# Kernel optimization log

Measured on AMD Instinct MI355X. Metric: run time of the kernel, lower is better.

## Reference

```python
import jax, jax.numpy as jnp
import numpy as np

OUT_HW = 224  # fixed by the dilation tensor built inside forward
K = 3         # kernel size


def _axis_terms(coords, size):
    """Bilinear interpolation terms along one axis.
    coords: float coordinates, any shape. Returns clipped int neighbor
    indices (i0, i1) and weights (w0, w1) with zero weight outside [0, size)."""
    c0 = jnp.floor(coords)
    f = coords - c0
    i0 = c0.astype(jnp.int32)
    i1 = i0 + 1
    w0 = (1.0 - f) * ((i0 >= 0) & (i0 < size)).astype(coords.dtype)
    w1 = f * ((i1 >= 0) & (i1 < size)).astype(coords.dtype)
    return jnp.clip(i0, 0, size - 1), jnp.clip(i1, 0, size - 1), w0, w1


def setup_inputs() -> dict:
    key = jax.random.key(0)
    k1, k2, k3 = jax.random.split(key, 3)
    B, C, H, W = 16, 3, 1024, 1024
    x = jax.random.normal(k1, (B, C, H, W), dtype=jnp.float32)
    # normalized sample coordinates in [-1, 1] per output row / column
    stride_h = jax.random.uniform(k2, (B, OUT_HW), dtype=jnp.float32, minval=-1.0, maxval=1.0)
    stride_w = jax.random.uniform(k3, (B, OUT_HW), dtype=jnp.float32, minval=-1.0, maxval=1.0)
    # fixed identity weight from __init__: center tap on channel diagonal
    w = np.zeros((3, 3, K, K), dtype=np.float32)
    for c in range(3):
        w[c, c, 1, 1] = 1.0
    return {"x": x, "stride_h": stride_h, "stride_w": stride_w, "weight": jnp.asarray(w)}


def reference(x, stride_h, stride_w, weight):
    B, C, H, W = x.shape
    dt = x.dtype
    # map normalized [-1,1] coords to pixel coords (as in forward)
    ch = (stride_h + 1.0) * (H - 1) * 0.5            # [B, outH]
    cw = (stride_w + 1.0) * (W - 1) * 0.5            # [B, outW]
    offs = (jnp.arange(K, dtype=dt) - (K - 1) / 2)   # dilation == 1 (built as ones in forward)
    ys = ch[:, :, None] + offs                       # [B, outH, K]
    xs = cw[:, :, None] + offs                       # [B, outW, K]

    yi0, yi1, wy0, wy1 = _axis_terms(ys, H)
    xi0, xi1, wx0, wx1 = _axis_terms(xs, W)

    # gather rows: [B, C, outH, K, W]
    gat_h = jax.vmap(lambda xb, idx: xb[:, idx, :])
    row = (wy0[:, None, :, :, None] * gat_h(x, yi0)
           + wy1[:, None, :, :, None] * gat_h(x, yi1))
    # gather cols: [B, C, outH, Kh, outW, Kw]
    gat_w = jax.vmap(lambda rb, idx: rb[..., idx])
    samp = (wx0[:, None, None, None] * gat_w(row, xi0)
            + wx1[:, None, None, None] * gat_w(row, xi1))
    # contract with (fixed) kernel: out[b,o,i,j]
    return jnp.einsum('bciujv,ocuv->boij', samp, weight)
```

## Files before the change

kernel.cpp:

```cpp
#include <hip/hip_runtime.h>

#define OH 224
#define OW 224
#define HH 1024
#define WW 1024
#define HW (HH * WW)

typedef __attribute__((address_space(3))) void lds_void_t;
typedef const __attribute__((address_space(1))) void g_void_t;

__global__ __launch_bounds__(256) void adaptive_sam_kernel(
    const float* __restrict__ x,
    const float* __restrict__ sh,
    const float* __restrict__ sw,
    const float* __restrict__ wgt,
    float* __restrict__ out,
    int B)
{
    __shared__ float lds[3 * 4 * WW];
    __shared__ float ws[81];

    const int tid = threadIdx.x;
    const int bi  = blockIdx.x;
    const int i   = bi % OH;
    const int b   = bi / OH;

    if (tid < 81) ws[tid] = wgt[tid];

    float chf = (sh[b * OH + i] + 1.0f) * ((HH - 1) * 0.5f);
    float cyf = floorf(chf); float fy = chf - cyf; int iy = (int)cyf;
    int rb = min(max(iy - 1, 0), HH - 4);

    {
        const int lane = tid & 63;
        const int wv   = tid >> 6;
        #pragma unroll
        for (int c = 0; c < 3; ++c) {
            const float* gbase = x + (size_t)(b * 3 + c) * HW + (size_t)rb * WW + wv * 1024;
            float* lbase = &lds[c * 4096 + wv * 1024];
            #pragma unroll
            for (int n = 0; n < 4; ++n) {
                const float* gp = gbase + n * 256 + lane * 4;
                __builtin_amdgcn_global_load_lds((g_void_t*)gp,
                                                 (lds_void_t*)(lbase + n * 256),
                                                 16, 0, 0);
            }
        }
    }
    __syncthreads();

    if (tid < OW) {
        const int j = tid;
        float cwf = (sw[b * OW + j] + 1.0f) * ((WW - 1) * 0.5f);
        float cxf = floorf(cwf); float fx = cwf - cxf; int ix = (int)cxf;
        int cb = min(max(ix - 1, 0), WW - 4);

        float Wy[3][4], Wx[3][4];
        #pragma unroll
        for (int u = 0; u < 3; ++u) {
            int y0 = iy + u - 1, y1 = y0 + 1;
            float a0 = (1.0f - fy) * ((y0 >= 0 && y0 < HH) ? 1.0f : 0.0f);
            float a1 = fy          * ((y1 >= 0 && y1 < HH) ? 1.0f : 0.0f);
            int py0 = min(max(y0, 0), HH - 1) - rb;
            int py1 = min(max(y1, 0), HH - 1) - rb;

            int x0 = ix + u - 1, x1 = x0 + 1;
            float b0 = (1.0f - fx) * ((x0 >= 0 && x0 < WW) ? 1.0f : 0.0f);
            float b1 = fx          * ((x1 >= 0 && x1 < WW) ? 1.0f : 0.0f);
            int px0 = min(max(x0, 0), WW - 1) - cb;
            int px1 = min(max(x1, 0), WW - 1) - cb;

            #pragma unroll
            for (int p = 0; p < 4; ++p) {
                Wy[u][p] = (py0 == p ? a0 : 0.0f) + (py1 == p ? a1 : 0.0f);
                Wx[u][p] = (px0 == p ? b0 : 0.0f) + (px1 == p ? b1 : 0.0f);
            }
        }

        float acc0 = 0.0f, acc1 = 0.0f, acc2 = 0.0f;
        #pragma unroll
        for (int c = 0; c < 3; ++c) {
            float hx[4][3];
            #pragma unroll
            for (int r = 0; r < 4; ++r) {
                const float* lp = &lds[c * 4096 + r * 1024 + cb];
                float p0 = lp[0], p1 = lp[1], p2 = lp[2], p3 = lp[3];
                #pragma unroll
                for (int v = 0; v < 3; ++v)
                    hx[r][v] = Wx[v][0] * p0 + Wx[v][1] * p1
                             + Wx[v][2] * p2 + Wx[v][3] * p3;
            }
            #pragma unroll
            for (int u = 0; u < 3; ++u)
                #pragma unroll
                for (int v = 0; v < 3; ++v) {
                    float s = Wy[u][0] * hx[0][v] + Wy[u][1] * hx[1][v]
                            + Wy[u][2] * hx[2][v] + Wy[u][3] * hx[3][v];
                    int wi = c * 9 + u * 3 + v;
                    acc0 = fmaf(ws[wi],      s, acc0);
                    acc1 = fmaf(ws[27 + wi], s, acc1);
                    acc2 = fmaf(ws[54 + wi], s, acc2);
                }
        }

        size_t obase = (size_t)b * 3 * OH * OW + (size_t)i * OW + j;
        out[obase]                = acc0;
        out[obase + OH * OW]      = acc1;
        out[obase + 2 * OH * OW]  = acc2;
    }
}

extern "C" void kernel_launch(void* const* d_in, const int* in_sizes, int n_in,
                              void* d_out, int out_size, void* d_ws, size_t ws_size,
                              hipStream_t stream) {
    const float* x  = (const float*)d_in[0];
    const float* sh = (const float*)d_in[1];
    const float* sw = (const float*)d_in[2];
    const float* w  = (const float*)d_in[3];
    float* out = (float*)d_out;

    int B = in_sizes[1] / OH;
    dim3 grid(B * OH);
    adaptive_sam_kernel<<<grid, 256, 0, stream>>>(x, sh, sw, w, out, B);
}
```

Measured before the change: 263.1 us.

## Split input channels across blocks and accumulate outputs with atomics

Each block now handles one input channel for one output row, which triples the grid and cuts LDS use per block from 48KB to 16KB. The goal is higher occupancy and more loads in flight. In exchange the output must be zeroed with a memset and each block adds its partial sums with float atomics. That means more global write traffic, an extra launch, and a summation order that is no longer deterministic.

```diff
diff --git a/kernel.cpp b/kernel.cpp
--- a/kernel.cpp
+++ b/kernel.cpp
@@ -17,15 +17,19 @@
     float* __restrict__ out,
     int B)
 {
-    __shared__ float lds[3 * 4 * WW];
-    __shared__ float ws[81];
+    __shared__ float lds[4 * WW];
+    __shared__ float ws[27];
 
     const int tid = threadIdx.x;
-    const int bi  = blockIdx.x;
+    const int cin = blockIdx.x % 3;
+    const int bi  = blockIdx.x / 3;
     const int i   = bi % OH;
     const int b   = bi / OH;
 
-    if (tid < 81) ws[tid] = wgt[tid];
+    if (tid < 27) {
+        int o = tid / 9, uv = tid % 9;
+        ws[tid] = wgt[(o * 3 + cin) * 9 + uv];
+    }
 
     float chf = (sh[b * OH + i] + 1.0f) * ((HH - 1) * 0.5f);
     float cyf = floorf(chf); float fy = chf - cyf; int iy = (int)cyf;
@@ -34,17 +38,14 @@
     {
         const int lane = tid & 63;
         const int wv   = tid >> 6;
+        const float* gbase = x + (size_t)(b * 3 + cin) * HW + (size_t)rb * WW + wv * 1024;
+        float* lbase = &lds[wv * 1024];
         #pragma unroll
-        for (int c = 0; c < 3; ++c) {
-            const float* gbase = x + (size_t)(b * 3 + c) * HW + (size_t)rb * WW + wv * 1024;
-            float* lbase = &lds[c * 4096 + wv * 1024];
-            #pragma unroll
-            for (int n = 0; n < 4; ++n) {
-                const float* gp = gbase + n * 256 + lane * 4;
-                __builtin_amdgcn_global_load_lds((g_void_t*)gp,
-                                                 (lds_void_t*)(lbase + n * 256),
-                                                 16, 0, 0);
-            }
+        for (int n = 0; n < 4; ++n) {
+            const float* gp = gbase + n * 256 + lane * 4;
+            __builtin_amdgcn_global_load_lds((g_void_t*)gp,
+                                             (lds_void_t*)(lbase + n * 256),
+                                             16, 0, 0);
         }
     }
     __syncthreads();
@@ -77,36 +78,34 @@
             }
         }
 
+        float hx[4][3];
+        #pragma unroll
+        for (int r = 0; r < 4; ++r) {
+            const float* lp = &lds[r * 1024 + cb];
+            float p0 = lp[0], p1 = lp[1], p2 = lp[2], p3 = lp[3];
+            #pragma unroll
+            for (int v = 0; v < 3; ++v)
+                hx[r][v] = Wx[v][0] * p0 + Wx[v][1] * p1
+                         + Wx[v][2] * p2 + Wx[v][3] * p3;
+        }
+
         float acc0 = 0.0f, acc1 = 0.0f, acc2 = 0.0f;
         #pragma unroll
-        for (int c = 0; c < 3; ++c) {
-            float hx[4][3];
+        for (int u = 0; u < 3; ++u)
             #pragma unroll
-            for (int r = 0; r < 4; ++r) {
-                const float* lp = &lds[c * 4096 + r * 1024 + cb];
-                float p0 = lp[0], p1 = lp[1], p2 = lp[2], p3 = lp[3];
-                #pragma unroll
-                for (int v = 0; v < 3; ++v)
-                    hx[r][v] = Wx[v][0] * p0 + Wx[v][1] * p1
-                             + Wx[v][2] * p2 + Wx[v][3] * p3;
+            for (int v = 0; v < 3; ++v) {
+                float s = Wy[u][0] * hx[0][v] + Wy[u][1] * hx[1][v]
+                        + Wy[u][2] * hx[2][v] + Wy[u][3] * hx[3][v];
+                int wi = u * 3 + v;
+                acc0 = fmaf(ws[wi],      s, acc0);
+                acc1 = fmaf(ws[9 + wi],  s, acc1);
+                acc2 = fmaf(ws[18 + wi], s, acc2);
             }
-            #pragma unroll
-            for (int u = 0; u < 3; ++u)
-                #pragma unroll
-                for (int v = 0; v < 3; ++v) {
-                    float s = Wy[u][0] * hx[0][v] + Wy[u][1] * hx[1][v]
-                            + Wy[u][2] * hx[2][v] + Wy[u][3] * hx[3][v];
-                    int wi = c * 9 + u * 3 + v;
-                    acc0 = fmaf(ws[wi],      s, acc0);
-                    acc1 = fmaf(ws[27 + wi], s, acc1);
-                    acc2 = fmaf(ws[54 + wi], s, acc2);
-                }
-        }
 
         size_t obase = (size_t)b * 3 * OH * OW + (size_t)i * OW + j;
-        out[obase]                = acc0;
-        out[obase + OH * OW]      = acc1;
-        out[obase + 2 * OH * OW]  = acc2;
+        atomicAdd(&out[obase],               acc0);
+        atomicAdd(&out[obase + OH * OW],     acc1);
+        atomicAdd(&out[obase + 2 * OH * OW], acc2);
     }
 }
 
@@ -120,6 +119,9 @@
     float* out = (float*)d_out;
 
     int B = in_sizes[1] / OH;
-    dim3 grid(B * OH);
+
+    hipMemsetAsync(out, 0, (size_t)out_size * sizeof(float), stream);
+
+    dim3 grid(B * OH * 3);
     adaptive_sam_kernel<<<grid, 256, 0, stream>>>(x, sh, sw, w, out, B);
 }
```

After: 266.4 us. Within noise of the previous version (+1.3%).
